# Kernel tuning notes

Measured on AMD Instinct MI355X. Metric: run time of the kernel, lower is better.

## Reference

```python
import jax, jax.numpy as jnp
import numpy as np

NUM_GROUPS = 32
EPS = 1e-6


def setup_inputs() -> dict:
    key = jax.random.key(0)
    ks = jax.random.split(key, 6)
    b, c, H, W = 4, 512, 64, 64
    scale = 1.0 / np.sqrt(c)
    return {
        "x": jax.random.normal(ks[0], (b, c, H, W), dtype=jnp.float32),
        "gn_w": jnp.ones((c,), jnp.float32),
        "gn_b": jnp.zeros((c,), jnp.float32),
        "wq": jax.random.normal(ks[1], (c, c), jnp.float32) * scale,
        "bq": jnp.zeros((c,), jnp.float32),
        "wk": jax.random.normal(ks[2], (c, c), jnp.float32) * scale,
        "bk": jnp.zeros((c,), jnp.float32),
        "wv": jax.random.normal(ks[3], (c, c), jnp.float32) * scale,
        "bv": jnp.zeros((c,), jnp.float32),
        "wp": jax.random.normal(ks[4], (c, c), jnp.float32) * scale,
        "bp": jnp.zeros((c,), jnp.float32),
    }


def _group_norm(x, gamma, beta):
    b, c, H, W = x.shape
    xg = x.reshape(b, NUM_GROUPS, c // NUM_GROUPS, H, W)
    mean = xg.mean(axis=(2, 3, 4), keepdims=True)
    var = xg.var(axis=(2, 3, 4), keepdims=True)
    xn = (xg - mean) * jax.lax.rsqrt(var + EPS)
    xn = xn.reshape(b, c, H, W)
    return xn * gamma[None, :, None, None] + beta[None, :, None, None]


def reference(x, gn_w, gn_b, wq, bq, wk, bk, wv, bv, wp, bp):
    b, c, H, W = x.shape
    h = _group_norm(x, gn_w, gn_b)  # (b,c,H,W)
    hf = h.reshape(b, c, H * W)  # (b,c,n)
    # 1x1 convs == per-pixel linear maps; weight layout [out,in]
    q = jnp.einsum('oc,bcn->bno', wq, hf) + bq  # (b,n,c)
    k = jnp.einsum('oc,bcn->bon', wk, hf) + bk[None, :, None]  # (b,c,n)
    v = jnp.einsum('oc,bcn->bon', wv, hf) + bv[None, :, None]  # (b,c,n)
    attn = jnp.einsum('bnc,bcm->bnm', q, k) * (int(c) ** (-0.5))
    attn = jax.nn.softmax(attn, axis=2)  # softmax over keys m
    # A = v @ attn^T  -> (b,c,n) where A[:, :, n] = sum_m v[:,:,m] attn[n,m]
    A = jnp.einsum('bcm,bnm->bcn', v, attn)
    A = jnp.einsum('oc,bcn->bon', wp, A) + bp[None, :, None]
    return x + A.reshape(b, c, H, W)
```

## Files before the change

### kernel.cpp

```cpp
#include <hip/hip_runtime.h>

#define BATCH 4
#define CCH 512
#define NPIX 4096
#define NGRP 32
#define GSZ 16
#define GN_EPS 1e-6f

typedef __attribute__((ext_vector_type(8))) short short8;
typedef __attribute__((ext_vector_type(8))) unsigned short ushort8;
typedef __attribute__((ext_vector_type(4))) unsigned short ushort4v;
typedef __attribute__((ext_vector_type(4))) float f32x4;

__device__ inline unsigned short f2bf(float f) {
  unsigned u = __float_as_uint(f);
  unsigned r = u + 0x7fffu + ((u >> 16) & 1u);
  return (unsigned short)(r >> 16);
}
__device__ inline float bf2f(unsigned short us) {
  return __uint_as_float(((unsigned)us) << 16);
}

__global__ __launch_bounds__(256) void gn_stats(const float* __restrict__ x,
                                                float* __restrict__ stats) {
  int bg = blockIdx.x;
  const f32x4* base = (const f32x4*)(x + (size_t)bg * (GSZ * NPIX));
  float s = 0.f, ss = 0.f;
  const int n4 = GSZ * NPIX / 4;
  for (int i = threadIdx.x; i < n4; i += 256) {
    f32x4 v = base[i];
    s += v.x + v.y + v.z + v.w;
    ss += v.x * v.x + v.y * v.y + v.z * v.z + v.w * v.w;
  }
  for (int off = 32; off > 0; off >>= 1) {
    s += __shfl_xor(s, off, 64);
    ss += __shfl_xor(ss, off, 64);
  }
  __shared__ float rs[4], rss[4];
  int lane = threadIdx.x & 63, wid = threadIdx.x >> 6;
  if (lane == 0) { rs[wid] = s; rss[wid] = ss; }
  __syncthreads();
  if (threadIdx.x == 0) {
    float S = rs[0] + rs[1] + rs[2] + rs[3];
    float SS = rss[0] + rss[1] + rss[2] + rss[3];
    const float inv = 1.f / (float)(GSZ * NPIX);
    float mean = S * inv;
    float var = SS * inv - mean * mean;
    stats[bg * 2] = mean;
    stats[bg * 2 + 1] = rsqrtf(var + GN_EPS);
  }
}

__global__ __launch_bounds__(256) void gn_apply_t(const float* __restrict__ x,
                                                  const float* __restrict__ stats,
                                                  const float* __restrict__ gw,
                                                  const float* __restrict__ gb,
                                                  unsigned short* __restrict__ hT) {
  __shared__ float tile[64][65];
  int b = blockIdx.z, c0 = blockIdx.y * 64, n0 = blockIdx.x * 64;
  int t = threadIdx.x;
  int tc4 = t & 15, tr = t >> 4;
  const float* xb = x + ((size_t)b * CCH + c0) * NPIX + n0;
#pragma unroll
  for (int j = 0; j < 4; ++j) {
    int row = tr + j * 16;
    int c = c0 + row;
    float mean = stats[((size_t)b * NGRP + (c >> 4)) * 2];
    float rstd = stats[((size_t)b * NGRP + (c >> 4)) * 2 + 1];
    float ga = gw[c] * rstd;
    float be = gb[c] - mean * ga;
    f32x4 v = *(const f32x4*)(xb + (size_t)row * NPIX + tc4 * 4);
    tile[row][tc4 * 4 + 0] = v.x * ga + be;
    tile[row][tc4 * 4 + 1] = v.y * ga + be;
    tile[row][tc4 * 4 + 2] = v.z * ga + be;
    tile[row][tc4 * 4 + 3] = v.w * ga + be;
  }
  __syncthreads();
  int cc = t & 7, nr = t >> 3;
  unsigned short* outp = hT + ((size_t)b * NPIX + n0) * CCH + c0;
#pragma unroll
  for (int j = 0; j < 2; ++j) {
    int n = nr + j * 32;
    ushort8 pk;
#pragma unroll
    for (int i = 0; i < 8; ++i) pk[i] = f2bf(tile[cc * 8 + i][n]);
    *(ushort8*)(outp + (size_t)n * CCH + cc * 8) = pk;
  }
}

__global__ __launch_bounds__(256) void f32_to_bf16(const float* __restrict__ src,
                                                   unsigned short* __restrict__ dst,
                                                   int n4) {
  int i = blockIdx.x * 256 + threadIdx.x;
  if (i < n4) {
    f32x4 v = ((const f32x4*)src)[i];
    ushort4v o;
    o.x = f2bf(v.x); o.y = f2bf(v.y); o.z = f2bf(v.z); o.w = f2bf(v.w);
    ((ushort4v*)dst)[i] = o;
  }
}

template <int BIAS_MODE, int OUT_BF16, int RESID, int SWZ>
__global__ __launch_bounds__(256, 2) void gemm_bt(
    const unsigned short* __restrict__ A, const unsigned short* __restrict__ B,
    void* __restrict__ Cv, const float* __restrict__ bias,
    const float* __restrict__ resid, int M, int N, int K, int lda, int ldb,
    int ldc, long sA, long sB, long sC, long sR, float scale) {
  __shared__ __align__(16) unsigned short lA[128][40];
  __shared__ __align__(16) unsigned short lB[128][40];
  const int t = threadIdx.x;
  const int lane = t & 63, w = t >> 6;
  const int wr = w >> 1, wc = w & 1;
  const int fr = lane & 15, kg = lane >> 4;

  unsigned orig = blockIdx.x + gridDim.x * (blockIdx.y + gridDim.y * blockIdx.z);
  unsigned nwg = gridDim.x * gridDim.y * gridDim.z;
  unsigned tid = (orig & 7) * (nwg >> 3) + (orig >> 3);
  int mt, ntl, bz;
  if (SWZ == 2) {
    unsigned bx = tid % gridDim.x, r = tid / gridDim.x;
    ntl = (int)bx;
    mt = (int)(r % gridDim.y);
    bz = (int)(r / gridDim.y);
  } else {
    unsigned bx = tid % gridDim.x, r = tid / gridDim.x;
    mt = (int)bx;
    ntl = (int)(r % gridDim.y);
    bz = (int)(r / gridDim.y);
  }
  const int m0 = mt * 128, n0 = ntl * 128;

  const unsigned short* Abz = A + (long)bz * sA;
  const unsigned short* Bbz = B + (long)bz * sB;
  const int srow = t >> 1, skc = (t & 1) * 16;
  const unsigned short* gA = Abz + (size_t)(m0 + srow) * lda + skc;
  const unsigned short* gB = Bbz + (size_t)(n0 + srow) * ldb + skc;

  short8 a0X = *(const short8*)(gA);
  short8 a1X = *(const short8*)(gA + 8);
  short8 b0X = *(const short8*)(gB);
  short8 b1X = *(const short8*)(gB + 8);
  short8 a0Y = *(const short8*)(gA + 32);
  short8 a1Y = *(const short8*)(gA + 40);
  short8 b0Y = *(const short8*)(gB + 32);
  short8 b1Y = *(const short8*)(gB + 40);

  f32x4 acc[4][4];
  const f32x4 zero = {0.f, 0.f, 0.f, 0.f};
#pragma unroll
  for (int m = 0; m < 4; ++m)
#pragma unroll
    for (int n = 0; n < 4; ++n) acc[m][n] = zero;

  const int NT = K >> 5;
#define COMPUTE()                                                             \
  do {                                                                        \
    short8 af[4], bfr[4];                                                     \
    _Pragma("unroll") for (int m = 0; m < 4; ++m) af[m] =                     \
        *(const short8*)&lA[wr * 64 + m * 16 + fr][kg * 8];                   \
    _Pragma("unroll") for (int n = 0; n < 4; ++n) bfr[n] =                    \
        *(const short8*)&lB[wc * 64 + n * 16 + fr][kg * 8];                   \
    _Pragma("unroll") for (int m = 0; m < 4; ++m)                             \
        _Pragma("unroll") for (int n = 0; n < 4; ++n) acc[m][n] =             \
            __builtin_amdgcn_mfma_f32_16x16x32_bf16(af[m], bfr[n],            \
                                                    acc[m][n], 0, 0, 0);      \
  } while (0)

  for (int it = 0; it < NT; it += 2) {
    __syncthreads();
    *(short8*)&lA[srow][skc] = a0X;
    *(short8*)&lA[srow][skc + 8] = a1X;
    *(short8*)&lB[srow][skc] = b0X;
    *(short8*)&lB[srow][skc + 8] = b1X;
    if (it + 2 < NT) {
      a0X = *(const short8*)(gA + (it + 2) * 32);
      a1X = *(const short8*)(gA + (it + 2) * 32 + 8);
      b0X = *(const short8*)(gB + (it + 2) * 32);
      b1X = *(const short8*)(gB + (it + 2) * 32 + 8);
    }
    __syncthreads();
    COMPUTE();
    __syncthreads();
    *(short8*)&lA[srow][skc] = a0Y;
    *(short8*)&lA[srow][skc + 8] = a1Y;
    *(short8*)&lB[srow][skc] = b0Y;
    *(short8*)&lB[srow][skc + 8] = b1Y;
    if (it + 3 < NT) {
      a0Y = *(const short8*)(gA + (it + 3) * 32);
      a1Y = *(const short8*)(gA + (it + 3) * 32 + 8);
      b0Y = *(const short8*)(gB + (it + 3) * 32);
      b1Y = *(const short8*)(gB + (it + 3) * 32 + 8);
    }
    __syncthreads();
    COMPUTE();
  }
#undef COMPUTE

  const int rowbase = m0 + wr * 64 + kg * 4;
  const int colbase = n0 + wc * 64 + fr;
#pragma unroll
  for (int m = 0; m < 4; ++m) {
#pragma unroll
    for (int n = 0; n < 4; ++n) {
      int col = colbase + n * 16;
#pragma unroll
      for (int r = 0; r < 4; ++r) {
        int row = rowbase + m * 16 + r;
        float v = acc[m][n][r] * scale;
        if (BIAS_MODE == 1) v += bias[row];
        if (BIAS_MODE == 2) v += bias[col];
        if (RESID) v += resid[(size_t)bz * sR + (size_t)row * ldc + col];
        size_t idx = (size_t)bz * sC + (size_t)row * ldc + col;
        if (OUT_BF16)
          ((unsigned short*)Cv)[idx] = f2bf(v);
        else
          ((float*)Cv)[idx] = v;
      }
    }
  }
}

__global__ __launch_bounds__(512, 2) void attn_fused(
    const unsigned short* __restrict__ qg, const unsigned short* __restrict__ kg2,
    const unsigned short* __restrict__ vg, unsigned short* __restrict__ og,
    float scale) {
  __shared__ __align__(16) unsigned short Qs[64 * 520];
  __shared__ __align__(16) unsigned short Ks[2][17408];
  __shared__ __align__(16) unsigned short Ps[64 * 136];
  __shared__ float lred[2][32][4];
  __shared__ float linv[64];

  const int t = threadIdx.x;
  const int lane = t & 63;
  const int wid = t >> 6;
  const int wq = wid >> 2, wc = wid & 3;
  const int fr = lane & 15, kgp = lane >> 4;

  unsigned logical = ((unsigned)blockIdx.x & 7) * 32 + ((unsigned)blockIdx.x >> 3);
  const int bz = (int)(logical >> 6), qt = (int)(logical & 63);
  const size_t BS = (size_t)NPIX * CCH;
  const unsigned short* qb = qg + (size_t)bz * BS + (size_t)qt * 64 * CCH;
  const unsigned short* kb = kg2 + (size_t)bz * BS;
  const unsigned short* vb = vg + (size_t)bz * BS;

  {
    const int row = t >> 3, c0 = (t & 7) * 64;
    const unsigned short* src = qb + (size_t)row * CCH + c0;
#pragma unroll
    for (int i = 0; i < 8; ++i)
      *(short8*)&Qs[row * 520 + c0 + i * 8] = *(const short8*)(src + i * 8);
  }

  const int krow = t >> 2, kseg = t & 3;
  const unsigned short* gK = kb + (size_t)krow * CCH + kseg * 32;
  const int kldsoff = krow * 136 + kseg * 32;
  const unsigned short* gV = vb + (size_t)t * NPIX;
  const int vldsbase = t * 32;
  const int vxor = t & 3;

  short8 R0, R1, R2, R3;
#define LOADK(mt_, cc_)                                                       \
  do { const unsigned short* g = gK + (size_t)(mt_) * (128 * CCH) + (cc_) * 128; \
    R0 = *(const short8*)(g); R1 = *(const short8*)(g + 8);                   \
    R2 = *(const short8*)(g + 16); R3 = *(const short8*)(g + 24); } while (0)
#define LOADV(mt_, vc_)                                                       \
  do { const unsigned short* g = gV + (mt_) * 128 + (vc_) * 32;               \
    R0 = *(const short8*)(g); R1 = *(const short8*)(g + 8);                   \
    R2 = *(const short8*)(g + 16); R3 = *(const short8*)(g + 24); } while (0)
#define WRITEK(buf_)                                                          \
  do { unsigned short* d = &Ks[buf_][kldsoff];                                \
    *(short8*)(d) = R0; *(short8*)(d + 8) = R1;                               \
    *(short8*)(d + 16) = R2; *(short8*)(d + 24) = R3; } while (0)
#define WRITEV(buf_)                                                          \
  do { unsigned short* d = &Ks[buf_][vldsbase];                               \
    *(short8*)(d + ((0 ^ vxor) * 8)) = R0; *(short8*)(d + ((1 ^ vxor) * 8)) = R1; \
    *(short8*)(d + ((2 ^ vxor) * 8)) = R2; *(short8*)(d + ((3 ^ vxor) * 8)) = R3; } while (0)

  f32x4 oa[2][8];
  const f32x4 zero = {0.f, 0.f, 0.f, 0.f};
#pragma unroll
  for (int i = 0; i < 2; ++i)
#pragma unroll
    for (int j = 0; j < 8; ++j) oa[i][j] = zero;
  f32x4 racc0 = zero, racc1 = zero;

  LOADK(0, 0);
  for (int mt = 0; mt < 32; ++mt) {
    f32x4 s00 = zero, s01 = zero, s10 = zero, s11 = zero;
#pragma unroll
    for (int ph = 0; ph < 8; ++ph) {
      const int buf = ph & 1;
      if (ph < 4) WRITEK(buf); else WRITEV(buf);
      if (ph < 3) { LOADK(mt, ph + 1); }
      else if (ph == 3) { LOADV(mt, 0); }
      else if (ph < 7) { LOADV(mt, ph - 3); }
      else { if (mt + 1 < 32) LOADK(mt + 1, 0); }
      __syncthreads();
      if (ph < 4) {
#pragma unroll
        for (int kk = 0; kk < 4; ++kk) {
          short8 a0 = *(const short8*)&Qs[(wq * 32 + fr) * 520 + ph * 128 + kk * 32 + kgp * 8];
          short8 a1 = *(const short8*)&Qs[(wq * 32 + 16 + fr) * 520 + ph * 128 + kk * 32 + kgp * 8];
          short8 b0 = *(const short8*)&Ks[buf][(wc * 32 + fr) * 136 + kk * 32 + kgp * 8];
          short8 b1 = *(const short8*)&Ks[buf][(wc * 32 + 16 + fr) * 136 + kk * 32 + kgp * 8];
          s00 = __builtin_amdgcn_mfma_f32_16x16x32_bf16(a0, b0, s00, 0, 0, 0);
          s01 = __builtin_amdgcn_mfma_f32_16x16x32_bf16(a0, b1, s01, 0, 0, 0);
          s10 = __builtin_amdgcn_mfma_f32_16x16x32_bf16(a1, b0, s10, 0, 0, 0);
          s11 = __builtin_amdgcn_mfma_f32_16x16x32_bf16(a1, b1, s11, 0, 0, 0);
        }
        if (ph == 3) {
          f32x4 p00, p01, p10, p11;
#pragma unroll
          for (int r = 0; r < 4; ++r) {
            p00[r] = __expf(s00[r] * scale);
            p01[r] = __expf(s01[r] * scale);
            p10[r] = __expf(s10[r] * scale);
            p11[r] = __expf(s11[r] * scale);
          }
          f32x4 rs0 = p00 + p01, rs1 = p10 + p11;
#pragma unroll
          for (int off = 1; off <= 8; off <<= 1) {
#pragma unroll
            for (int r = 0; r < 4; ++r) {
              rs0[r] += __shfl_xor(rs0[r], off, 64);
              rs1[r] += __shfl_xor(rs1[r], off, 64);
            }
          }
          racc0 += rs0;
          racc1 += rs1;
#pragma unroll
          for (int r = 0; r < 4; ++r) {
            Ps[(wq * 32 + kgp * 4 + r) * 136 + wc * 32 + fr] = f2bf(p00[r]);
            Ps[(wq * 32 + kgp * 4 + r) * 136 + wc * 32 + 16 + fr] = f2bf(p01[r]);
            Ps[(wq * 32 + 16 + kgp * 4 + r) * 136 + wc * 32 + fr] = f2bf(p10[r]);
            Ps[(wq * 32 + 16 + kgp * 4 + r) * 136 + wc * 32 + 16 + fr] = f2bf(p11[r]);
          }
        }
      } else {
        const int vc = ph - 4;
        short8 pa0 = *(const short8*)&Ps[(wq * 32 + fr) * 136 + vc * 32 + kgp * 8];
        short8 pa1 = *(const short8*)&Ps[(wq * 32 + 16 + fr) * 136 + vc * 32 + kgp * 8];
#pragma unroll
        for (int fb = 0; fb < 8; ++fb) {
          const int c = wc * 128 + fb * 16 + fr;
          short8 bv = *(const short8*)&Ks[buf][c * 32 + ((kgp ^ (c & 3)) * 8)];
          oa[0][fb] = __builtin_amdgcn_mfma_f32_16x16x32_bf16(pa0, bv, oa[0][fb], 0, 0, 0);
          oa[1][fb] = __builtin_amdgcn_mfma_f32_16x16x32_bf16(pa1, bv, oa[1][fb], 0, 0, 0);
        }
      }
    }
  }
#undef LOADK
#undef LOADV
#undef WRITEK
#undef WRITEV

  if (fr == 0) {
#pragma unroll
    for (int r = 0; r < 4; ++r) {
      lred[wq][kgp * 4 + r][wc] = racc0[r];
      lred[wq][16 + kgp * 4 + r][wc] = racc1[r];
    }
  }
  __syncthreads();
  if (t < 64) {
    float s = lred[t >> 5][t & 31][0] + lred[t >> 5][t & 31][1] +
              lred[t >> 5][t & 31][2] + lred[t >> 5][t & 31][3];
    linv[t] = 1.f / s;
  }
  __syncthreads();
#pragma unroll
  for (int i = 0; i < 2; ++i) {
    f32x4 li = *(const f32x4*)&linv[wq * 32 + i * 16 + kgp * 4];
#pragma unroll
    for (int fb = 0; fb < 8; ++fb) {
#pragma unroll
      for (int r = 0; r < 4; ++r)
        Qs[(wq * 32 + i * 16 + kgp * 4 + r) * 520 + wc * 128 + fb * 16 + fr] =
            f2bf(oa[i][fb][r] * li[r]);
    }
  }
  __syncthreads();
  {
    const int row = t >> 3, c0 = (t & 7) * 64;
    unsigned short* dst = og + (size_t)bz * BS + ((size_t)qt * 64 + row) * CCH + c0;
#pragma unroll
    for (int i = 0; i < 8; ++i)
      *(short8*)(dst + i * 8) = *(const short8*)&Qs[row * 520 + c0 + i * 8];
  }
}

extern "C" void kernel_launch(void* const* d_in, const int* in_sizes, int n_in,
                              void* d_out, int out_size, void* d_ws, size_t ws_size,
                              hipStream_t stream) {
  const float* x = (const float*)d_in[0];
  const float* gnw = (const float*)d_in[1];
  const float* gnb = (const float*)d_in[2];
  const float* wq = (const float*)d_in[3];
  const float* bq = (const float*)d_in[4];
  const float* wk = (const float*)d_in[5];
  const float* bk = (const float*)d_in[6];
  const float* wv = (const float*)d_in[7];
  const float* bv = (const float*)d_in[8];
  const float* wp = (const float*)d_in[9];
  const float* bp = (const float*)d_in[10];
  float* out = (float*)d_out;

  const size_t BS = (size_t)NPIX * CCH;

  char* ws = (char*)d_ws;
  float* stats = (float*)ws;
  unsigned short* hT = (unsigned short*)(ws + 1024);
  unsigned short* Abuf = hT;
  unsigned short* qb = hT + BATCH * BS;
  unsigned short* kTb = qb + BATCH * BS;
  unsigned short* vb = kTb + BATCH * BS;
  unsigned short* wqb = vb + BATCH * BS;
  unsigned short* wkb = wqb + CCH * CCH;
  unsigned short* wvb = wkb + CCH * CCH;
  unsigned short* wpb = wvb + CCH * CCH;
  size_t need = (size_t)((char*)(wpb + CCH * CCH) - ws);
  if (ws_size < need) return;

  f32_to_bf16<<<256, 256, 0, stream>>>(wq, wqb, CCH * CCH / 4);
  f32_to_bf16<<<256, 256, 0, stream>>>(wk, wkb, CCH * CCH / 4);
  f32_to_bf16<<<256, 256, 0, stream>>>(wv, wvb, CCH * CCH / 4);
  f32_to_bf16<<<256, 256, 0, stream>>>(wp, wpb, CCH * CCH / 4);

  gn_stats<<<BATCH * NGRP, 256, 0, stream>>>(x, stats);
  gn_apply_t<<<dim3(NPIX / 64, CCH / 64, BATCH), 256, 0, stream>>>(x, stats, gnw,
                                                                   gnb, hT);

  gemm_bt<2, 1, 0, 2><<<dim3(4, 32, BATCH), 256, 0, stream>>>(
      hT, wqb, qb, bq, nullptr, NPIX, CCH, CCH, CCH, CCH, CCH, (long)BS, 0,
      (long)BS, 0, 1.f);
  gemm_bt<2, 1, 0, 2><<<dim3(4, 32, BATCH), 256, 0, stream>>>(
      hT, wkb, kTb, bk, nullptr, NPIX, CCH, CCH, CCH, CCH, CCH, (long)BS, 0,
      (long)BS, 0, 1.f);
  gemm_bt<1, 1, 0, 0><<<dim3(4, 32, BATCH), 256, 0, stream>>>(
      wvb, hT, vb, bv, nullptr, CCH, NPIX, CCH, CCH, CCH, NPIX, 0, (long)BS,
      (long)BS, 0, 1.f);

  const float sscale = 0.044194173824159216f;
  attn_fused<<<BATCH * 64, 512, 0, stream>>>(qb, kTb, vb, Abuf, sscale);

  gemm_bt<1, 0, 1, 0><<<dim3(4, 32, BATCH), 256, 0, stream>>>(
      wpb, Abuf, out, bp, x, CCH, NPIX, CCH, CCH, CCH, NPIX, 0, (long)BS,
      (long)BS, (long)BS, 1.f);
}
```

Before: 340.5 us.

## Restructure fused attention with 256-key tiles, per-wave key split, swizzled LDS, double register prefetch

Rewrites the attention kernel's inner loop. Each step now processes 256 keys: every wave computes scores for all 64 queries against its own 32 keys, then owns 64 output channels in the PV product. This replaces the earlier 2x4 query/channel wave grid. Padded LDS rows are replaced by XOR swizzles, two register sets prefetch global chunks two phases ahead, and the barriers are raw s_barrier calls with setprio around the MFMA blocks. The exponent step is split across wave halves to overlap it with the V phases. This adds register pressure under launch_bounds(512,2) and makes the synchronization more complex.

```diff
diff --git a/kernel.cpp b/kernel.cpp
--- a/kernel.cpp
+++ b/kernel.cpp
@@ -221,172 +221,225 @@
 }
 
 __global__ __launch_bounds__(512, 2) void attn_fused(
-    const unsigned short* __restrict__ qg, const unsigned short* __restrict__ kg2,
+    const unsigned short* __restrict__ qg, const unsigned short* __restrict__ kgl,
     const unsigned short* __restrict__ vg, unsigned short* __restrict__ og,
     float scale) {
-  __shared__ __align__(16) unsigned short Qs[64 * 520];
-  __shared__ __align__(16) unsigned short Ks[2][17408];
-  __shared__ __align__(16) unsigned short Ps[64 * 136];
-  __shared__ float lred[2][32][4];
-  __shared__ float linv[64];
+  __shared__ __align__(16) unsigned short Qs[64 * 512];
+  __shared__ __align__(16) unsigned short Ck[2][256 * 64];
+  __shared__ __align__(16) unsigned short Ps[64 * 128];
 
   const int t = threadIdx.x;
-  const int lane = t & 63;
-  const int wid = t >> 6;
-  const int wq = wid >> 2, wc = wid & 3;
+  const int lane = t & 63, w = t >> 6;
   const int fr = lane & 15, kgp = lane >> 4;
 
   unsigned logical = ((unsigned)blockIdx.x & 7) * 32 + ((unsigned)blockIdx.x >> 3);
   const int bz = (int)(logical >> 6), qt = (int)(logical & 63);
   const size_t BS = (size_t)NPIX * CCH;
   const unsigned short* qb = qg + (size_t)bz * BS + (size_t)qt * 64 * CCH;
-  const unsigned short* kb = kg2 + (size_t)bz * BS;
+  const unsigned short* kb = kgl + (size_t)bz * BS;
   const unsigned short* vb = vg + (size_t)bz * BS;
 
+  const int krow = t >> 1;
+  const int khalf = (t & 1) * 32;
+  const int kswz = (krow & 7) << 3;
+  const int vswz = (t & 3) << 3;
+
+  short8 RX0, RX1, RX2, RX3, RY0, RY1, RY2, RY3;
+
+#define LOADCH(SET, mt2, sub2)                                                \
+  do {                                                                        \
+    if ((mt2) < 16) {                                                         \
+      const unsigned short* g;                                                \
+      if ((sub2) < 8)                                                         \
+        g = kb + (size_t)((mt2)*256 + krow) * CCH + (sub2)*64 + khalf;        \
+      else                                                                    \
+        g = vb + (size_t)t * NPIX + (mt2)*256 + ((sub2)-8) * 32;              \
+      SET##0 = *(const short8*)(g);                                           \
+      SET##1 = *(const short8*)(g + 8);                                       \
+      SET##2 = *(const short8*)(g + 16);                                      \
+      SET##3 = *(const short8*)(g + 24);                                      \
+    }                                                                         \
+  } while (0)
+
+#define WRITEK(BUF, SET)                                                      \
+  do {                                                                        \
+    unsigned short* d = &Ck[BUF][krow * 64];                                  \
+    *(short8*)(d + ((khalf + 0) ^ kswz)) = SET##0;                            \
+    *(short8*)(d + ((khalf + 8) ^ kswz)) = SET##1;                            \
+    *(short8*)(d + ((khalf + 16) ^ kswz)) = SET##2;                           \
+    *(short8*)(d + ((khalf + 24) ^ kswz)) = SET##3;                           \
+  } while (0)
+
+#define WRITEV(BUF, SET)                                                      \
+  do {                                                                        \
+    unsigned short* d = &Ck[BUF][t * 32];                                     \
+    *(short8*)(d + (0 ^ vswz)) = SET##0;                                      \
+    *(short8*)(d + (8 ^ vswz)) = SET##1;                                      \
+    *(short8*)(d + (16 ^ vswz)) = SET##2;                                     \
+    *(short8*)(d + (24 ^ vswz)) = SET##3;                                     \
+  } while (0)
+
+#define PHASE_BAR()                                                           \
+  do {                                                                        \
+    asm volatile("s_waitcnt lgkmcnt(0)" ::: "memory");                        \
+    __builtin_amdgcn_s_barrier();                                             \
+    __builtin_amdgcn_sched_barrier(0);                                        \
+  } while (0)
+
+  LOADCH(RX, 0, 0);
+  LOADCH(RY, 0, 1);
   {
     const int row = t >> 3, c0 = (t & 7) * 64;
     const unsigned short* src = qb + (size_t)row * CCH + c0;
+    const int sw = (row & 7) << 3;
 #pragma unroll
     for (int i = 0; i < 8; ++i)
-      *(short8*)&Qs[row * 520 + c0 + i * 8] = *(const short8*)(src + i * 8);
-  }
-
-  const int krow = t >> 2, kseg = t & 3;
-  const unsigned short* gK = kb + (size_t)krow * CCH + kseg * 32;
-  const int kldsoff = krow * 136 + kseg * 32;
-  const unsigned short* gV = vb + (size_t)t * NPIX;
-  const int vldsbase = t * 32;
-  const int vxor = t & 3;
-
-  short8 R0, R1, R2, R3;
-#define LOADK(mt_, cc_)                                                       \
-  do { const unsigned short* g = gK + (size_t)(mt_) * (128 * CCH) + (cc_) * 128; \
-    R0 = *(const short8*)(g); R1 = *(const short8*)(g + 8);                   \
-    R2 = *(const short8*)(g + 16); R3 = *(const short8*)(g + 24); } while (0)
-#define LOADV(mt_, vc_)                                                       \
-  do { const unsigned short* g = gV + (mt_) * 128 + (vc_) * 32;               \
-    R0 = *(const short8*)(g); R1 = *(const short8*)(g + 8);                   \
-    R2 = *(const short8*)(g + 16); R3 = *(const short8*)(g + 24); } while (0)
-#define WRITEK(buf_)                                                          \
-  do { unsigned short* d = &Ks[buf_][kldsoff];                                \
-    *(short8*)(d) = R0; *(short8*)(d + 8) = R1;                               \
-    *(short8*)(d + 16) = R2; *(short8*)(d + 24) = R3; } while (0)
-#define WRITEV(buf_)                                                          \
-  do { unsigned short* d = &Ks[buf_][vldsbase];                               \
-    *(short8*)(d + ((0 ^ vxor) * 8)) = R0; *(short8*)(d + ((1 ^ vxor) * 8)) = R1; \
-    *(short8*)(d + ((2 ^ vxor) * 8)) = R2; *(short8*)(d + ((3 ^ vxor) * 8)) = R3; } while (0)
-
-  f32x4 oa[2][8];
+      *(short8*)&Qs[row * 512 + ((c0 + i * 8) ^ sw)] = *(const short8*)(src + i * 8);
+  }
+
+  f32x4 s_acc[4][2], o_acc[4][4], racc[4];
   const f32x4 zero = {0.f, 0.f, 0.f, 0.f};
 #pragma unroll
-  for (int i = 0; i < 2; ++i)
-#pragma unroll
-    for (int j = 0; j < 8; ++j) oa[i][j] = zero;
-  f32x4 racc0 = zero, racc1 = zero;
-
-  LOADK(0, 0);
-  for (int mt = 0; mt < 32; ++mt) {
-    f32x4 s00 = zero, s01 = zero, s10 = zero, s11 = zero;
-#pragma unroll
-    for (int ph = 0; ph < 8; ++ph) {
-      const int buf = ph & 1;
-      if (ph < 4) WRITEK(buf); else WRITEV(buf);
-      if (ph < 3) { LOADK(mt, ph + 1); }
-      else if (ph == 3) { LOADV(mt, 0); }
-      else if (ph < 7) { LOADV(mt, ph - 3); }
-      else { if (mt + 1 < 32) LOADK(mt + 1, 0); }
-      __syncthreads();
-      if (ph < 4) {
-#pragma unroll
-        for (int kk = 0; kk < 4; ++kk) {
-          short8 a0 = *(const short8*)&Qs[(wq * 32 + fr) * 520 + ph * 128 + kk * 32 + kgp * 8];
-          short8 a1 = *(const short8*)&Qs[(wq * 32 + 16 + fr) * 520 + ph * 128 + kk * 32 + kgp * 8];
-          short8 b0 = *(const short8*)&Ks[buf][(wc * 32 + fr) * 136 + kk * 32 + kgp * 8];
-          short8 b1 = *(const short8*)&Ks[buf][(wc * 32 + 16 + fr) * 136 + kk * 32 + kgp * 8];
-          s00 = __builtin_amdgcn_mfma_f32_16x16x32_bf16(a0, b0, s00, 0, 0, 0);
-          s01 = __builtin_amdgcn_mfma_f32_16x16x32_bf16(a0, b1, s01, 0, 0, 0);
-          s10 = __builtin_amdgcn_mfma_f32_16x16x32_bf16(a1, b0, s10, 0, 0, 0);
-          s11 = __builtin_amdgcn_mfma_f32_16x16x32_bf16(a1, b1, s11, 0, 0, 0);
+  for (int i = 0; i < 4; ++i) {
+    s_acc[i][0] = zero; s_acc[i][1] = zero; racc[i] = zero;
+#pragma unroll
+    for (int n = 0; n < 4; ++n) o_acc[i][n] = zero;
+  }
+
+#define EXP_HALF(h)                                                           \
+  do {                                                                        \
+    if ((w >> 2) == (h)) {                                                    \
+      _Pragma("unroll") for (int i = 0; i < 4; ++i) {                         \
+        f32x4 p0, p1;                                                         \
+        _Pragma("unroll") for (int r = 0; r < 4; ++r) {                       \
+          p0[r] = __expf(s_acc[i][0][r] * scale);                             \
+          p1[r] = __expf(s_acc[i][1][r] * scale);                             \
+        }                                                                     \
+        f32x4 rs = p0 + p1;                                                   \
+        _Pragma("unroll") for (int off = 1; off <= 8; off <<= 1)              \
+            _Pragma("unroll") for (int r = 0; r < 4; ++r) rs[r] +=            \
+            __shfl_xor(rs[r], off, 64);                                       \
+        racc[i] += rs;                                                        \
+        _Pragma("unroll") for (int r = 0; r < 4; ++r) {                       \
+          int q = i * 16 + kgp * 4 + r;                                       \
+          int sw2 = (q & 7) << 3;                                             \
+          Ps[q * 128 + (((w & 3) * 32 + fr) ^ sw2)] = f2bf(p0[r]);            \
+          Ps[q * 128 + (((w & 3) * 32 + 16 + fr) ^ sw2)] = f2bf(p1[r]);       \
+        }                                                                     \
+        s_acc[i][0] = zero; s_acc[i][1] = zero;                               \
+      }                                                                       \
+    }                                                                         \
+  } while (0)
+
+  for (int mt = 0; mt < 16; ++mt) {
+#pragma unroll
+    for (int sub = 0; sub < 8; ++sub) {
+      const int buf = sub & 1;
+      if (buf == 0) { WRITEK(0, RX); LOADCH(RX, mt, sub + 2); }
+      else          { WRITEK(1, RY); LOADCH(RY, mt, sub + 2); }
+      PHASE_BAR();
+      __builtin_amdgcn_s_setprio(1);
+#pragma unroll
+      for (int kk = 0; kk < 2; ++kk) {
+        short8 a[4], b[2];
+#pragma unroll
+        for (int i = 0; i < 4; ++i) {
+          int q = i * 16 + fr;
+          a[i] = *(const short8*)&Qs[q * 512 +
+                 ((sub * 64 + kk * 32 + kgp * 8) ^ ((q & 7) << 3))];
         }
-        if (ph == 3) {
-          f32x4 p00, p01, p10, p11;
-#pragma unroll
-          for (int r = 0; r < 4; ++r) {
-            p00[r] = __expf(s00[r] * scale);
-            p01[r] = __expf(s01[r] * scale);
-            p10[r] = __expf(s10[r] * scale);
-            p11[r] = __expf(s11[r] * scale);
-          }
-          f32x4 rs0 = p00 + p01, rs1 = p10 + p11;
-#pragma unroll
-          for (int off = 1; off <= 8; off <<= 1) {
-#pragma unroll
-            for (int r = 0; r < 4; ++r) {
-              rs0[r] += __shfl_xor(rs0[r], off, 64);
-              rs1[r] += __shfl_xor(rs1[r], off, 64);
-            }
-          }
-          racc0 += rs0;
-          racc1 += rs1;
-#pragma unroll
-          for (int r = 0; r < 4; ++r) {
-            Ps[(wq * 32 + kgp * 4 + r) * 136 + wc * 32 + fr] = f2bf(p00[r]);
-            Ps[(wq * 32 + kgp * 4 + r) * 136 + wc * 32 + 16 + fr] = f2bf(p01[r]);
-            Ps[(wq * 32 + 16 + kgp * 4 + r) * 136 + wc * 32 + fr] = f2bf(p10[r]);
-            Ps[(wq * 32 + 16 + kgp * 4 + r) * 136 + wc * 32 + 16 + fr] = f2bf(p11[r]);
-          }
+#pragma unroll
+        for (int n = 0; n < 2; ++n) {
+          int ml = w * 32 + n * 16 + fr;
+          b[n] = *(const short8*)&Ck[buf][ml * 64 +
+                 ((kk * 32 + kgp * 8) ^ ((ml & 7) << 3))];
         }
-      } else {
-        const int vc = ph - 4;
-        short8 pa0 = *(const short8*)&Ps[(wq * 32 + fr) * 136 + vc * 32 + kgp * 8];
-        short8 pa1 = *(const short8*)&Ps[(wq * 32 + 16 + fr) * 136 + vc * 32 + kgp * 8];
-#pragma unroll
-        for (int fb = 0; fb < 8; ++fb) {
-          const int c = wc * 128 + fb * 16 + fr;
-          short8 bv = *(const short8*)&Ks[buf][c * 32 + ((kgp ^ (c & 3)) * 8)];
-          oa[0][fb] = __builtin_amdgcn_mfma_f32_16x16x32_bf16(pa0, bv, oa[0][fb], 0, 0, 0);
-          oa[1][fb] = __builtin_amdgcn_mfma_f32_16x16x32_bf16(pa1, bv, oa[1][fb], 0, 0, 0);
+#pragma unroll
+        for (int i = 0; i < 4; ++i) {
+          s_acc[i][0] = __builtin_amdgcn_mfma_f32_16x16x32_bf16(a[i], b[0], s_acc[i][0], 0, 0, 0);
+          s_acc[i][1] = __builtin_amdgcn_mfma_f32_16x16x32_bf16(a[i], b[1], s_acc[i][1], 0, 0, 0);
         }
       }
+      __builtin_amdgcn_s_setprio(0);
     }
-  }
-#undef LOADK
-#undef LOADV
+    EXP_HALF(0);
+#pragma unroll
+    for (int vph = 0; vph < 8; ++vph) {
+      const int sub = 8 + vph, buf = sub & 1;
+      if (vph == 4) {
+        PHASE_BAR();
+        EXP_HALF(1);
+      }
+      if (buf == 0) { WRITEV(0, RX); LOADCH(RX, mt + ((sub + 2) >> 4), (sub + 2) & 15); }
+      else          { WRITEV(1, RY); LOADCH(RY, mt + ((sub + 2) >> 4), (sub + 2) & 15); }
+      PHASE_BAR();
+      __builtin_amdgcn_s_setprio(1);
+      {
+        short8 a[4], b[4];
+#pragma unroll
+        for (int i = 0; i < 4; ++i) {
+          int q = i * 16 + fr;
+          a[i] = *(const short8*)&Ps[q * 128 +
+                 (((vph & 3) * 32 + kgp * 8) ^ ((q & 7) << 3))];
+        }
+#pragma unroll
+        for (int n = 0; n < 4; ++n) {
+          int c = w * 64 + n * 16 + fr;
+          b[n] = *(const short8*)&Ck[buf][c * 32 + ((kgp * 8) ^ ((c & 3) << 3))];
+        }
+#pragma unroll
+        for (int i = 0; i < 4; ++i)
+#pragma unroll
+          for (int n = 0; n < 4; ++n)
+            o_acc[i][n] = __builtin_amdgcn_mfma_f32_16x16x32_bf16(a[i], b[n], o_acc[i][n], 0, 0, 0);
+      }
+      __builtin_amdgcn_s_setprio(0);
+    }
+  }
+#undef LOADCH
 #undef WRITEK
 #undef WRITEV
-
+#undef EXP_HALF
+
+  __syncthreads();
+  float* lred = (float*)Ps;
+  float* linv = lred + 512;
   if (fr == 0) {
 #pragma unroll
-    for (int r = 0; r < 4; ++r) {
-      lred[wq][kgp * 4 + r][wc] = racc0[r];
-      lred[wq][16 + kgp * 4 + r][wc] = racc1[r];
-    }
+    for (int i = 0; i < 4; ++i)
+#pragma unroll
+      for (int r = 0; r < 4; ++r)
+        lred[(i * 16 + kgp * 4 + r) * 8 + w] = racc[i][r];
   }
   __syncthreads();
   if (t < 64) {
-    float s = lred[t >> 5][t & 31][0] + lred[t >> 5][t & 31][1] +
-              lred[t >> 5][t & 31][2] + lred[t >> 5][t & 31][3];
+    float s = 0.f;
+#pragma unroll
+    for (int j = 0; j < 8; ++j) s += lred[t * 8 + j];
     linv[t] = 1.f / s;
   }
   __syncthreads();
 #pragma unroll
-  for (int i = 0; i < 2; ++i) {
-    f32x4 li = *(const f32x4*)&linv[wq * 32 + i * 16 + kgp * 4];
-#pragma unroll
-    for (int fb = 0; fb < 8; ++fb) {
-#pragma unroll
-      for (int r = 0; r < 4; ++r)
-        Qs[(wq * 32 + i * 16 + kgp * 4 + r) * 520 + wc * 128 + fb * 16 + fr] =
-            f2bf(oa[i][fb][r] * li[r]);
+  for (int i = 0; i < 4; ++i) {
+    f32x4 li = *(const f32x4*)&linv[i * 16 + kgp * 4];
+#pragma unroll
+    for (int n = 0; n < 4; ++n) {
+#pragma unroll
+      for (int r = 0; r < 4; ++r) {
+        int q = i * 16 + kgp * 4 + r;
+        int col = w * 64 + n * 16 + fr;
+        Qs[q * 512 + (col ^ ((q & 7) << 3))] = f2bf(o_acc[i][n][r] * li[r]);
+      }
     }
   }
   __syncthreads();
   {
     const int row = t >> 3, c0 = (t & 7) * 64;
+    const int sw = (row & 7) << 3;
     unsigned short* dst = og + (size_t)bz * BS + ((size_t)qt * 64 + row) * CCH + c0;
 #pragma unroll
     for (int i = 0; i < 8; ++i)
-      *(short8*)(dst + i * 8) = *(const short8*)&Qs[row * 520 + c0 + i * 8];
+      *(short8*)(dst + i * 8) = *(const short8*)&Qs[row * 512 + ((c0 + i * 8) ^ sw)];
   }
 }
 
```

New measurement: 381.3 us. 12.0% more time.
